# Kernel optimization log

Hardware: AMD Instinct MI355X
Metric: run time of the kernel (lower is better)

Reference implementation:

```python
import jax, jax.numpy as jnp
import numpy as np

B, S, D, F, E = 4, 4096, 1024, 2048, 8


def setup_inputs() -> dict:
    key = jax.random.key(0)
    ks = jax.random.split(key, 8)
    x = jax.random.normal(ks[0], (B, S, D), dtype=jnp.float32)
    # router (nn.Linear(d_model, num_experts))
    Wr = jax.random.normal(ks[1], (D, E), dtype=jnp.float32) * 0.02
    br = jnp.zeros((E,), dtype=jnp.float32)
    # stacked per-expert MLP params: Linear(D,F) -> GELU -> Linear(F,D)
    W1 = jax.random.normal(ks[2], (E, D, F), dtype=jnp.float32) * (1.0 / np.sqrt(D))
    b1 = jnp.zeros((E, F), dtype=jnp.float32)
    W2 = jax.random.normal(ks[3], (E, F, D), dtype=jnp.float32) * (1.0 / np.sqrt(F))
    b2 = jnp.zeros((E, D), dtype=jnp.float32)
    return {"x": x, "Wr": Wr, "br": br, "W1": W1, "b1": b1, "W2": W2, "b2": b2}


def reference(x, Wr, br, W1, b1, W2, b2):
    # router: softmax over experts, top-1 selection
    logits = jnp.einsum("bsd,de->bse", x, Wr) + br          # [B,S,E]
    probs = jax.nn.softmax(logits, axis=-1)
    expert_weights = jnp.max(probs, axis=-1)                  # [B,S]
    expert_indices = jnp.argmax(probs, axis=-1)               # [B,S]

    num_experts = W1.shape[0]
    out = jnp.zeros_like(x)
    # loop over the small fixed set of experts (structurally distinct weights)
    for e in range(num_experts):
        h = jax.nn.gelu(jnp.einsum("bsd,df->bsf", x, W1[e]) + b1[e], approximate=False)
        y = jnp.einsum("bsf,fd->bsd", h, W2[e]) + b2[e]
        out = jnp.where((expert_indices == e)[..., None], y, out)

    return out * expert_weights[..., None]
```

## Files before the change

kernel.cpp:

```cpp
#include <hip/hip_runtime.h>
#include <hip/hip_bf16.h>


typedef __attribute__((ext_vector_type(8))) short short8;
typedef __attribute__((ext_vector_type(4))) float f32x4;

struct __align__(8) us4 { unsigned short x, y, z, w; };

__device__ __forceinline__ void gload16(const void* g, void* l) {
  __builtin_amdgcn_global_load_lds(
      (const __attribute__((address_space(1))) unsigned int*)g,
      (__attribute__((address_space(3))) unsigned int*)l, 16, 0, 0);
}

__device__ __forceinline__ unsigned short f2b(float f) {
  union { float f; unsigned u; } v; v.f = f;
  unsigned r = v.u + 0x7FFFu + ((v.u >> 16) & 1u);
  return (unsigned short)(r >> 16);
}

__global__ __launch_bounds__(256) void router_logits(
    const float* __restrict__ x, const float* __restrict__ Wr,
    const float* __restrict__ br, float* __restrict__ wts,
    int* __restrict__ eidx, unsigned short* __restrict__ xb)
{
  const int lane = threadIdx.x & 63;
  const int wid  = threadIdx.x >> 6;
  const int t = blockIdx.x * 4 + wid;

  const float4* x4 = (const float4*)(x + (size_t)t * 1024);
  float acc[8];
#pragma unroll
  for (int e = 0; e < 8; ++e) acc[e] = 0.f;
#pragma unroll
  for (int i = 0; i < 4; ++i) {
    float4 v = x4[lane + 64 * i];
    const int d = (lane + 64 * i) * 4;
    const float* wr = Wr + (size_t)d * 8;
    float xs[4] = {v.x, v.y, v.z, v.w};
    us4 o;
    o.x = f2b(v.x); o.y = f2b(v.y); o.z = f2b(v.z); o.w = f2b(v.w);
    *(us4*)(xb + (size_t)t * 1024 + (size_t)(lane + 64 * i) * 4) = o;
#pragma unroll
    for (int j = 0; j < 4; ++j) {
      float4 w0 = *(const float4*)(wr + j * 8);
      float4 w1 = *(const float4*)(wr + j * 8 + 4);
      acc[0] += xs[j] * w0.x; acc[1] += xs[j] * w0.y;
      acc[2] += xs[j] * w0.z; acc[3] += xs[j] * w0.w;
      acc[4] += xs[j] * w1.x; acc[5] += xs[j] * w1.y;
      acc[6] += xs[j] * w1.z; acc[7] += xs[j] * w1.w;
    }
  }
#pragma unroll
  for (int e = 0; e < 8; ++e) {
    float v = acc[e];
#pragma unroll
    for (int m = 32; m; m >>= 1) v += __shfl_xor(v, m, 64);
    acc[e] = v;
  }
  if (lane == 0) {
    float lg[8];
#pragma unroll
    for (int e = 0; e < 8; ++e) lg[e] = acc[e] + br[e];
    float mx = lg[0]; int bi = 0;
#pragma unroll
    for (int e = 1; e < 8; ++e) if (lg[e] > mx) { mx = lg[e]; bi = e; }
    float s = 0.f;
#pragma unroll
    for (int e = 0; e < 8; ++e) s += expf(lg[e] - mx);
    wts[t]  = 1.0f / s;
    eidx[t] = bi;
  }
}

__global__ __launch_bounds__(256) void bucketize(
    const int* __restrict__ eidx, int* __restrict__ cnt, int* __restrict__ list)
{
  __shared__ int lcnt[8], base[8];
  const int tid = threadIdx.x;
  if (tid < 8) lcnt[tid] = 0;
  __syncthreads();
  const int t = blockIdx.x * 256 + tid;
  const int e = eidx[t];
  const int lpos = atomicAdd(&lcnt[e], 1);
  __syncthreads();
  if (tid < 8) base[tid] = atomicAdd(&cnt[tid], lcnt[tid]);
  __syncthreads();
  list[e * 16384 + base[e] + lpos] = t;
}

__global__ __launch_bounds__(256) void transpose_cvt(
    const float* __restrict__ W, unsigned short* __restrict__ Wt, int K, int N)
{
  __shared__ float tl[64][65];
  const int e = blockIdx.z;
  const float* Wp = W + (size_t)e * K * N;
  unsigned short* Wtp = Wt + (size_t)e * K * N;
  const int k0 = blockIdx.y * 64, n0 = blockIdx.x * 64;
  const int r = threadIdx.x >> 4, c4 = (threadIdx.x & 15) * 4;
#pragma unroll
  for (int i = 0; i < 4; ++i) {
    float4 v = *(const float4*)(Wp + (size_t)(k0 + r + i * 16) * N + n0 + c4);
    tl[r + i * 16][c4 + 0] = v.x; tl[r + i * 16][c4 + 1] = v.y;
    tl[r + i * 16][c4 + 2] = v.z; tl[r + i * 16][c4 + 3] = v.w;
  }
  __syncthreads();
#pragma unroll
  for (int i = 0; i < 4; ++i) {
    const int n = r + i * 16;
    us4 o;
    o.x = f2b(tl[c4 + 0][n]); o.y = f2b(tl[c4 + 1][n]);
    o.z = f2b(tl[c4 + 2][n]); o.w = f2b(tl[c4 + 3][n]);
    *(us4*)(Wtp + (size_t)(n0 + n) * K + k0 + c4) = o;
  }
}

template <int K, int N, int EPI, int LOGNB>
__global__ __launch_bounds__(512, 4) void gemm_moe8(
    const unsigned short* __restrict__ A,
    const unsigned short* __restrict__ Bt,
    const float* __restrict__ bias,
    const int* __restrict__ cnt, const int* __restrict__ list,
    const float* __restrict__ wts, void* __restrict__ outp)
{
  constexpr int NT = K / 32;
  constexpr int NB = 1 << LOGNB;
  extern __shared__ char lds[];
  int*   tok_s = (int*)(lds + 49152);
  float* wt_s  = (float*)(lds + 50176);

  const int q = gridDim.x >> 3;
  const int p = ((int)blockIdx.x & 7) * q + ((int)blockIdx.x >> 3);
  int e = -1, pre = 0, cnte = 0, loc = p;
#pragma unroll
  for (int i = 0; i < 8; ++i) {
    const int c = cnt[i];
    const int bl = ((c + 255) >> 8) << LOGNB;
    if (e < 0) {
      if (loc < bl) { e = i; cnte = c; }
      else { loc -= bl; pre += c; }
    }
  }
  if (e < 0) return;
  const int row0 = (loc >> LOGNB) << 8;
  const int n0   = (loc & (NB - 1)) << 7;

  const int tid = threadIdx.x;
  const int lane = tid & 63, wid = tid >> 6;
  const int wr = wid >> 2, wc = wid & 3;
  const int l15 = lane & 15;

  if (tid < 256) {
    const int s = row0 + tid;
    if (s < cnte) {
      const int t = list[e * 16384 + s];
      tok_s[tid] = t;
      wt_s[tid]  = (EPI == 2) ? wts[t] : 0.f;
    } else { tok_s[tid] = 0; wt_s[tid] = 0.f; }
  }
  __syncthreads();

  const int srow = tid >> 2;
  const int gch  = ((tid & 3) ^ ((srow >> 1) & 3)) * 8;
  const unsigned short* aG0;
  const unsigned short* aG1;
  if (EPI == 1) {
    aG0 = A + (size_t)tok_s[srow] * K + gch;
    aG1 = A + (size_t)tok_s[128 + srow] * K + gch;
  } else {
    aG0 = A + (size_t)min(pre + row0 + srow, 16383) * K + gch;
    aG1 = A + (size_t)min(pre + row0 + 128 + srow, 16383) * K + gch;
  }
  const unsigned short* bG0 = Bt + ((size_t)e * N + n0 + srow) * K + gch;

  const int xo = (((lane >> 4) ^ ((l15 >> 1) & 3)) << 4);
  const char* aB = lds + wr * 8192 + l15 * 64 + xo;
  const char* bB = lds + 32768 + wc * 2048 + l15 * 64 + xo;

  f32x4 acc[8][2];
#pragma unroll
  for (int m = 0; m < 8; ++m)
#pragma unroll
    for (int n = 0; n < 2; ++n) acc[m][n] = (f32x4){0.f, 0.f, 0.f, 0.f};

#define STG_A(S, T) do { \
    char* d_ = lds + (S) * 16384 + (wid << 10); \
    gload16(aG0 + (size_t)(T) * 32, d_); \
    gload16(aG1 + (size_t)(T) * 32, d_ + 8192); } while (0)
#define STG_B(S, T) do { \
    char* d_ = lds + 32768 + (S) * 8192 + (wid << 10); \
    gload16(bG0 + (size_t)(T) * 32, d_); } while (0)

  STG_A(0, 0); STG_B(0, 0);
  asm volatile("s_waitcnt vmcnt(0)" ::: "memory");
  __builtin_amdgcn_s_barrier();

  short8 aF[8], bF[2];
#pragma unroll 1
  for (int T = 0; T < NT; ++T) {
    const int buf = T & 1;
    const int Ts  = (T + 1 < NT) ? T + 1 : NT - 1;
    STG_A(buf ^ 1, Ts);
    STG_B(buf ^ 1, Ts);
    const char* aT = aB + buf * 16384;
    const char* bT = bB + buf * 8192;
#pragma unroll
    for (int m = 0; m < 8; ++m) aF[m] = *(const short8*)(aT + m * 1024);
#pragma unroll
    for (int n = 0; n < 2; ++n) bF[n] = *(const short8*)(bT + n * 1024);
    asm volatile("s_waitcnt lgkmcnt(0)" ::: "memory");
    __builtin_amdgcn_sched_barrier(0);
    __builtin_amdgcn_s_setprio(1);
#pragma unroll
    for (int m = 0; m < 8; ++m)
#pragma unroll
      for (int n = 0; n < 2; ++n)
        acc[m][n] = __builtin_amdgcn_mfma_f32_16x16x32_bf16(
            aF[m], bF[n], acc[m][n], 0, 0, 0);
    __builtin_amdgcn_s_setprio(0);
    __builtin_amdgcn_sched_barrier(0);
    asm volatile("s_waitcnt vmcnt(0)" ::: "memory");
    __builtin_amdgcn_s_barrier();
  }
#undef STG_A
#undef STG_B

  const int cRow0 = wr * 128 + ((lane >> 4) << 2);
  const int cColB = n0 + wc * 32 + l15;
  float bv[2];
#pragma unroll
  for (int nf = 0; nf < 2; ++nf) bv[nf] = bias[e * N + cColB + nf * 16];

  if (EPI == 1) {
    unsigned short* H = (unsigned short*)outp;
#pragma unroll
    for (int m = 0; m < 8; ++m)
#pragma unroll
      for (int r = 0; r < 4; ++r) {
        const int sl = cRow0 + m * 16 + r;
        if (row0 + sl < cnte) {
          const size_t rp = (size_t)(pre + row0 + sl) * N + cColB;
#pragma unroll
          for (int nf = 0; nf < 2; ++nf) {
            float v = acc[m][nf][r] + bv[nf];
            float u = 1.5957691216f * v * (1.0f + 0.044715f * v * v);
            float ex = __expf(u);
            float th = 1.0f - 2.0f / (ex + 1.0f);
            v = 0.5f * v * (1.0f + th);
            H[rp + nf * 16] = f2b(v);
          }
        }
      }
  } else {
    float* O = (float*)outp;
#pragma unroll
    for (int m = 0; m < 8; ++m)
#pragma unroll
      for (int r = 0; r < 4; ++r) {
        const int sl = cRow0 + m * 16 + r;
        if (row0 + sl < cnte) {
          const size_t rp = (size_t)tok_s[sl] * N + cColB;
          const float w = wt_s[sl];
#pragma unroll
          for (int nf = 0; nf < 2; ++nf)
            O[rp + nf * 16] = (acc[m][nf][r] + bv[nf]) * w;
        }
      }
  }
}

extern "C" void kernel_launch(void* const* d_in, const int* in_sizes, int n_in,
                              void* d_out, int out_size, void* d_ws, size_t ws_size,
                              hipStream_t stream) {
  const float* x  = (const float*)d_in[0];
  const float* Wr = (const float*)d_in[1];
  const float* br = (const float*)d_in[2];
  const float* W1 = (const float*)d_in[3];
  const float* b1 = (const float*)d_in[4];
  const float* W2 = (const float*)d_in[5];
  const float* b2 = (const float*)d_in[6];

  char* ws = (char*)d_ws;
  int*   cnt  = (int*)ws;
  float* wts  = (float*)(ws + 256);
  int*   eidx = (int*)(ws + 256 + 64 * 1024);
  int*   list = (int*)(ws + 256 + 128 * 1024);
  unsigned short* xb  = (unsigned short*)(ws + 1024 * 1024);
  unsigned short* w1t = xb  + (size_t)16384 * 1024;
  unsigned short* w2t = w1t + (size_t)8 * 2048 * 1024;
  unsigned short* h   = w2t + (size_t)8 * 1024 * 2048;

  constexpr int LDS_BYTES = 51200;
  hipFuncSetAttribute((const void*)gemm_moe8<1024, 2048, 1, 4>,
                      hipFuncAttributeMaxDynamicSharedMemorySize, LDS_BYTES);
  hipFuncSetAttribute((const void*)gemm_moe8<2048, 1024, 2, 3>,
                      hipFuncAttributeMaxDynamicSharedMemorySize, LDS_BYTES);

  hipMemsetAsync(cnt, 0, 32, stream);
  router_logits<<<dim3(4096), 256, 0, stream>>>(x, Wr, br, wts, eidx, xb);
  bucketize<<<dim3(64), 256, 0, stream>>>(eidx, cnt, list);
  transpose_cvt<<<dim3(32, 16, 8), 256, 0, stream>>>(W1, w1t, 1024, 2048);
  transpose_cvt<<<dim3(16, 32, 8), 256, 0, stream>>>(W2, w2t, 2048, 1024);
  gemm_moe8<1024, 2048, 1, 4><<<dim3(71 * 16), 512, LDS_BYTES, stream>>>(
      xb, w1t, b1, cnt, list, wts, (void*)h);
  gemm_moe8<2048, 1024, 2, 3><<<dim3(71 * 8), 512, LDS_BYTES, stream>>>(
      h, w2t, b2, cnt, list, wts, d_out);
}
```

Measured before the change: 345.6 us.

## Triple-buffer GEMM LDS stages with prefetch distance two

Moves the MoE GEMM main loop from double to triple buffering in LDS. Each iteration prefetches the tile two steps ahead and waits only for older loads (vmcnt(3)) rather than draining all outstanding global loads before the barrier. The loop is unrolled by three so buffer indices are compile-time constants. This lets global-to-LDS latency overlap more MFMA work. The cost is LDS per block rising from about 50 KB to about 74 KB, which may reduce how many blocks fit per CU given launch_bounds(512,4).

```diff
diff --git a/kernel.cpp b/kernel.cpp
--- a/kernel.cpp
+++ b/kernel.cpp
@@ -126,8 +126,8 @@
   constexpr int NT = K / 32;
   constexpr int NB = 1 << LOGNB;
   extern __shared__ char lds[];
-  int*   tok_s = (int*)(lds + 49152);
-  float* wt_s  = (float*)(lds + 50176);
+  int*   tok_s = (int*)(lds + 73728);
+  float* wt_s  = (float*)(lds + 74752);
 
   const int q = gridDim.x >> 3;
   const int p = ((int)blockIdx.x & 7) * q + ((int)blockIdx.x >> 3);
@@ -175,7 +175,7 @@
 
   const int xo = (((lane >> 4) ^ ((l15 >> 1) & 3)) << 4);
   const char* aB = lds + wr * 8192 + l15 * 64 + xo;
-  const char* bB = lds + 32768 + wc * 2048 + l15 * 64 + xo;
+  const char* bB = lds + 49152 + wc * 2048 + l15 * 64 + xo;
 
   f32x4 acc[8][2];
 #pragma unroll
@@ -188,42 +188,50 @@
     gload16(aG0 + (size_t)(T) * 32, d_); \
     gload16(aG1 + (size_t)(T) * 32, d_ + 8192); } while (0)
 #define STG_B(S, T) do { \
-    char* d_ = lds + 32768 + (S) * 8192 + (wid << 10); \
+    char* d_ = lds + 49152 + (S) * 8192 + (wid << 10); \
     gload16(bG0 + (size_t)(T) * 32, d_); } while (0)
 
+#define TILE_BODY(T, SR, SS) do { \
+    const int Ts_ = ((T) + 2 < NT) ? (T) + 2 : NT - 1;    \
+    STG_A(SS, Ts_); \
+    STG_B(SS, Ts_); \
+    const char* aT = aB + (SR) * 16384; \
+    const char* bT = bB + (SR) * 8192; \
+    short8 aF[8], bF[2]; \
+    _Pragma("unroll") \
+    for (int m_ = 0; m_ < 8; ++m_) aF[m_] = *(const short8*)(aT + m_ * 1024); \
+    _Pragma("unroll") \
+    for (int n_ = 0; n_ < 2; ++n_) bF[n_] = *(const short8*)(bT + n_ * 1024); \
+    asm volatile("s_waitcnt lgkmcnt(0)" ::: "memory"); \
+    __builtin_amdgcn_sched_barrier(0); \
+    __builtin_amdgcn_s_setprio(1); \
+    _Pragma("unroll") \
+    for (int m_ = 0; m_ < 8; ++m_) \
+      _Pragma("unroll") \
+      for (int n_ = 0; n_ < 2; ++n_) \
+        acc[m_][n_] = __builtin_amdgcn_mfma_f32_16x16x32_bf16( \
+            aF[m_], bF[n_], acc[m_][n_], 0, 0, 0); \
+    __builtin_amdgcn_s_setprio(0); \
+    __builtin_amdgcn_sched_barrier(0); \
+    asm volatile("s_waitcnt vmcnt(3)" ::: "memory");    \
+    __builtin_amdgcn_s_barrier(); \
+  } while (0)
+
   STG_A(0, 0); STG_B(0, 0);
-  asm volatile("s_waitcnt vmcnt(0)" ::: "memory");
+  STG_A(1, 1); STG_B(1, 1);
+  asm volatile("s_waitcnt vmcnt(3)" ::: "memory");
   __builtin_amdgcn_s_barrier();
 
-  short8 aF[8], bF[2];
 #pragma unroll 1
-  for (int T = 0; T < NT; ++T) {
-    const int buf = T & 1;
-    const int Ts  = (T + 1 < NT) ? T + 1 : NT - 1;
-    STG_A(buf ^ 1, Ts);
-    STG_B(buf ^ 1, Ts);
-    const char* aT = aB + buf * 16384;
-    const char* bT = bB + buf * 8192;
-#pragma unroll
-    for (int m = 0; m < 8; ++m) aF[m] = *(const short8*)(aT + m * 1024);
-#pragma unroll
-    for (int n = 0; n < 2; ++n) bF[n] = *(const short8*)(bT + n * 1024);
-    asm volatile("s_waitcnt lgkmcnt(0)" ::: "memory");
-    __builtin_amdgcn_sched_barrier(0);
-    __builtin_amdgcn_s_setprio(1);
-#pragma unroll
-    for (int m = 0; m < 8; ++m)
-#pragma unroll
-      for (int n = 0; n < 2; ++n)
-        acc[m][n] = __builtin_amdgcn_mfma_f32_16x16x32_bf16(
-            aF[m], bF[n], acc[m][n], 0, 0, 0);
-    __builtin_amdgcn_s_setprio(0);
-    __builtin_amdgcn_sched_barrier(0);
-    asm volatile("s_waitcnt vmcnt(0)" ::: "memory");
-    __builtin_amdgcn_s_barrier();
-  }
+  for (int T = 0; T < NT; T += 3) {
+    TILE_BODY(T, 0, 2);
+    if (T + 1 < NT) TILE_BODY(T + 1, 1, 0);
+    if (T + 2 < NT) TILE_BODY(T + 2, 2, 1);
+  }
+#undef TILE_BODY
 #undef STG_A
 #undef STG_B
+  asm volatile("s_waitcnt vmcnt(0)" ::: "memory");
 
   const int cRow0 = wr * 128 + ((lane >> 4) << 2);
   const int cColB = n0 + wc * 32 + l15;
@@ -290,7 +298,7 @@
   unsigned short* w2t = w1t + (size_t)8 * 2048 * 1024;
   unsigned short* h   = w2t + (size_t)8 * 1024 * 2048;
 
-  constexpr int LDS_BYTES = 51200;
+  constexpr int LDS_BYTES = 75776;
   hipFuncSetAttribute((const void*)gemm_moe8<1024, 2048, 1, 4>,
                       hipFuncAttributeMaxDynamicSharedMemorySize, LDS_BYTES);
   hipFuncSetAttribute((const void*)gemm_moe8<2048, 1024, 2, 3>,
```

New measurement: 321.2 us. -7.1%, faster.
